# Kernel tuning notes

Hardware: AMD Instinct MI355X
Metric: run time of the kernel (lower is better)

The kernel has to match this reference:

```python
import jax, jax.numpy as jnp
import numpy as np

# config dims (see shape_source)
NO = 8        # Max_Object
NT = 32       # Max_Time
C = 512       # feat_dims
VD = 1024     # visual_dim
RD = 300      # self.nfeat (relation word-vector dim)
H = 4         # headnum
B = 8         # batch
No = NT * 2 * NO      # 512 object-graph nodes
Nr = NT * NO * NO     # 2048 relation-graph nodes


def _glorot(key, shape):
    fan_in = shape[0]
    return jax.random.normal(key, shape, dtype=jnp.float32) / np.sqrt(fan_in)


def setup_inputs() -> dict:
    key = jax.random.key(0)
    ks = jax.random.split(key, 18)
    inp = {
        "Ao": jax.random.uniform(ks[0], (B, No, No), dtype=jnp.float32),
        "srco": jax.random.normal(ks[1], (B, 1, 1, No, VD), dtype=jnp.float32),
        "Ar": jax.random.uniform(ks[2], (B, Nr, Nr), dtype=jnp.float32),
        "srcr": jax.random.normal(ks[3], (B, 1, 1, Nr, RD), dtype=jnp.float32),
        # GraphConvolution weights: gcl_o/gcl2_o and gcl_r/gcl2_r
        "Wo1": _glorot(ks[4], (VD, 1024)),
        "Wo2": _glorot(ks[5], (1024, C)),
        "Wr1": _glorot(ks[6], (RD, 1024)),
        "Wr2": _glorot(ks[7], (1024, C)),
        # MultiHeadAttention (e2n) projections
        "Wq": _glorot(ks[8], (C, C)), "bq": jnp.zeros((C,), jnp.float32),
        "Wk": _glorot(ks[9], (C, C)), "bk": jnp.zeros((C,), jnp.float32),
        "Wv": _glorot(ks[10], (C, C)), "bv": jnp.zeros((C,), jnp.float32),
        "Wp": _glorot(ks[11], (C, C)), "bp": jnp.zeros((C,), jnp.float32),
        # e2n_embed: Linear(2C -> C)
        "We": _glorot(ks[12], (2 * C, C)), "be": jnp.zeros((C,), jnp.float32),
    }
    return inp


def _gcn2(A, x, W1, W2):
    """Two stacked GraphConvolution layers with self-loops: relu((A+I) @ x @ W).
    A: (b,N,N), x: (b,N,Din). Vectorized over batch (torch code loops per-sample)."""
    eye = jnp.eye(A.shape[-1], dtype=A.dtype)
    Ah = A + eye
    h = jax.nn.relu(jnp.einsum('bij,bjd->bid', Ah, x @ W1))
    return jax.nn.relu(jnp.einsum('bij,bjd->bid', Ah, h @ W2))


def _mha(x, Wq, bq, Wk, bk, Wv, bv, Wp, bp):
    """Standard multi-head self-attention. x: (Bseg, S, C)."""
    Bs, S, _ = x.shape
    dh = C // H
    q = (x @ Wq + bq).reshape(Bs, S, H, dh)
    k = (x @ Wk + bk).reshape(Bs, S, H, dh)
    v = (x @ Wv + bv).reshape(Bs, S, H, dh)
    attn = jax.nn.softmax(jnp.einsum('bqhd,bkhd->bhqk', q, k) / np.sqrt(dh), axis=-1)
    o = jnp.einsum('bhqk,bkhd->bqhd', attn, v).reshape(Bs, S, C)
    return o @ Wp + bp


def _forward(Ao, srco, Ar, srcr, Wo1, Wo2, Wr1, Wr2,
             Wq, bq, Wk, bk, Wv, bv, Wp, bp, We, be):
    b = Ao.shape[0]
    # object-graph GCN (torch loops over batch; vectorized here)
    xo = srco[:, 0, 0, :, :VD]                       # (b, No, VD)
    srco_gcn = _gcn2(Ao, xo, Wo1, Wo2)               # (b, No, C)
    out_gcn_o = srco_gcn.reshape(b, NT, 2 * NO, C)
    # relation-graph GCN
    xr = srcr[:, 0, 0]                               # (b, Nr, RD)
    srcr_gcn = _gcn2(Ar, xr, Wr1, Wr2)               # (b, Nr, C)
    out_gcn_r = srcr_gcn.reshape(b, NT, NO * NO, C)
    # compute_e2n: segment-wise MHA over NO-token windows (torch loops over NO)
    r = out_gcn_r.reshape(b * NT, NO, NO, C)
    seg_a = r.reshape(b * NT * NO, NO, C)                      # rows of NOxNO grid
    a = _mha(seg_a, Wq, bq, Wk, bk, Wv, bv, Wp, bp).mean(axis=1)
    a = a.reshape(b * NT, NO, C)
    seg_o = jnp.swapaxes(r, 1, 2).reshape(b * NT * NO, NO, C)  # cols (permute 0,2,1,3)
    o = _mha(seg_o, Wq, bq, Wk, bk, Wv, bv, Wp, bp).mean(axis=1)
    o = o.reshape(b * NT, NO, C)
    tmp = jnp.concatenate([a, o], axis=1)                      # (b*NT, 2*NO, C)
    cat = jnp.concatenate([tmp, out_gcn_o.reshape(b * NT, 2 * NO, C)], axis=-1)
    out_e2n = cat @ We + be
    return out_e2n.reshape(b, NT, 2 * NO, C)


def reference(Ao, srco, Ar, srcr, Wo1, Wo2, Wr1, Wr2,
              Wq, bq, Wk, bk, Wv, bv, Wp, bp, We, be):
    return _forward(Ao, srco, Ar, srcr, Wo1, Wo2, Wr1, Wr2,
                    Wq, bq, Wk, bk, Wv, bv, Wp, bp, We, be)
```

## Files before the change

### kernel.cpp

```cpp
#include <hip/hip_runtime.h>
#include <hip/hip_bf16.h>


typedef __attribute__((ext_vector_type(4))) float f32x4;
typedef __attribute__((ext_vector_type(8))) short bf16x8s;

#define TILE 128
#define BKK 32
#define LDSS 40
#define LDSL 32

#if __has_builtin(__builtin_amdgcn_global_load_lds)
#define HAVE_GLL 1
#else
#define HAVE_GLL 0
#endif

__device__ inline void gll16(const __hip_bfloat16* g, __hip_bfloat16* l) {
#if HAVE_GLL
    __builtin_amdgcn_global_load_lds(
        (const __attribute__((address_space(1))) void*)g,
        (__attribute__((address_space(3))) void*)l,
        16, 0, 0);
#endif
}

__device__ inline void split2(float a, float b, unsigned& h, unsigned& l) {
    __hip_bfloat16 ha = __float2bfloat16(a), hb = __float2bfloat16(b);
    float ra = __bfloat162float(ha), rb = __bfloat162float(hb);
    __hip_bfloat16 la = __float2bfloat16(a - ra), lb = __float2bfloat16(b - rb);
    unsigned short uha = *(unsigned short*)&ha, uhb = *(unsigned short*)&hb;
    unsigned short ula = *(unsigned short*)&la, ulb = *(unsigned short*)&lb;
    h = (unsigned)uha | ((unsigned)uhb << 16);
    l = (unsigned)ula | ((unsigned)ulb << 16);
}

__device__ inline void splitw(float v, unsigned short& h, unsigned short& l) {
    __hip_bfloat16 hb = __float2bfloat16(v);
    __hip_bfloat16 lb = __float2bfloat16(v - __bfloat162float(hb));
    h = *(unsigned short*)&hb;
    l = *(unsigned short*)&lb;
}

__device__ inline void swz_block(int& bx, int& by, int& bz) {
    int gx = gridDim.x, gy = gridDim.y;
    int nwg = gx * gy * gridDim.z;
    int flat = bx + gx * (by + gy * bz);
    int cpx = nwg >> 3;
    int w = (flat & 7) * cpx + (flat >> 3);
    bx = w % gx;
    int t = w / gx;
    by = t % gy;
    bz = t / gy;
}

__global__ __launch_bounds__(256) void gemm_planes(
    const __hip_bfloat16* __restrict__ Aph, const __hip_bfloat16* __restrict__ Apl,
    long long sA, int lda,
    const __hip_bfloat16* __restrict__ BTh, const __hip_bfloat16* __restrict__ BTl,
    long long sBT, int ldbt,
    void* __restrict__ D, __hip_bfloat16* __restrict__ Dl_, long long sD, int ldd,
    const float* __restrict__ addN, long long sAddN, int ldaddN,
    const __hip_bfloat16* __restrict__ addTh, const __hip_bfloat16* __restrict__ addTl,
    long long sAddT, int ldaddT,
    const float* __restrict__ bias,
    int K, int relu, int outMode)
{
    __shared__ __hip_bfloat16 Ah[TILE * LDSL], Al[TILE * LDSL];
    __shared__ __hip_bfloat16 Bh[TILE * LDSL], Bl[TILE * LDSL];

    int bx = blockIdx.x, by = blockIdx.y, bz = blockIdx.z;
    swz_block(bx, by, bz);

    const int tid  = threadIdx.x;
    const int lane = tid & 63;
    const int wave = tid >> 6;
    const int wm   = (wave >> 1) * 64;
    const int wn   = (wave & 1) * 64;
    const int row0 = by * TILE;
    const int col0 = bx * TILE;
    const int b    = bz;

    const __hip_bfloat16* Abh = Aph + (size_t)b * sA;
    const __hip_bfloat16* Abl = Apl + (size_t)b * sA;
    const __hip_bfloat16* Bbh = BTh + (size_t)b * sBT;
    const __hip_bfloat16* Bbl = BTl + (size_t)b * sBT;

    f32x4 acc[4][4];
#pragma unroll
    for (int i = 0; i < 4; ++i)
#pragma unroll
        for (int j = 0; j < 4; ++j) acc[i][j] = (f32x4){0.f, 0.f, 0.f, 0.f};

    const int quad = lane >> 4;
    const int l16  = lane & 15;

    const int m0  = wave * 16 + (lane >> 2);
    const int m1  = (wave + 4) * 16 + (lane >> 2);
    const int sl  = lane & 3;
    const int kq0 = sl ^ ((m0 >> 1) & 3);
    const int kq1 = sl ^ ((m1 >> 1) & 3);
    const size_t gA0 = (size_t)(row0 + m0) * lda + kq0 * 8;
    const size_t gA1 = (size_t)(row0 + m1) * lda + kq1 * 8;
    const size_t gB0 = (size_t)(col0 + m0) * ldbt + kq0 * 8;
    const size_t gB1 = (size_t)(col0 + m1) * ldbt + kq1 * 8;
    const int ldsc0 = wave * 512;
    const int ldsc1 = (wave + 4) * 512;

    for (int k0 = 0; k0 < K; k0 += BKK) {
        __syncthreads();
#if HAVE_GLL
        gll16(Abh + gA0 + k0, &Ah[ldsc0]);
        gll16(Abh + gA1 + k0, &Ah[ldsc1]);
        gll16(Abl + gA0 + k0, &Al[ldsc0]);
        gll16(Abl + gA1 + k0, &Al[ldsc1]);
        gll16(Bbh + gB0 + k0, &Bh[ldsc0]);
        gll16(Bbh + gB1 + k0, &Bh[ldsc1]);
        gll16(Bbl + gB0 + k0, &Bl[ldsc0]);
        gll16(Bbl + gB1 + k0, &Bl[ldsc1]);
#else
        *(uint4*)(&Ah[m0 * LDSL + sl * 8]) = *(const uint4*)(Abh + gA0 + k0);
        *(uint4*)(&Ah[m1 * LDSL + sl * 8]) = *(const uint4*)(Abh + gA1 + k0);
        *(uint4*)(&Al[m0 * LDSL + sl * 8]) = *(const uint4*)(Abl + gA0 + k0);
        *(uint4*)(&Al[m1 * LDSL + sl * 8]) = *(const uint4*)(Abl + gA1 + k0);
        *(uint4*)(&Bh[m0 * LDSL + sl * 8]) = *(const uint4*)(Bbh + gB0 + k0);
        *(uint4*)(&Bh[m1 * LDSL + sl * 8]) = *(const uint4*)(Bbh + gB1 + k0);
        *(uint4*)(&Bl[m0 * LDSL + sl * 8]) = *(const uint4*)(Bbl + gB0 + k0);
        *(uint4*)(&Bl[m1 * LDSL + sl * 8]) = *(const uint4*)(Bbl + gB1 + k0);
#endif
        __syncthreads();

        bf16x8s bhf[4], blf[4];
#pragma unroll
        for (int nt = 0; nt < 4; ++nt) {
            int r = wn + nt * 16 + l16;
            int ss = (quad ^ ((r >> 1) & 3)) * 8;
            bhf[nt] = *(const bf16x8s*)(&Bh[r * LDSL + ss]);
            blf[nt] = *(const bf16x8s*)(&Bl[r * LDSL + ss]);
        }
#pragma unroll
        for (int mt = 0; mt < 4; ++mt) {
            int r = wm + mt * 16 + l16;
            int ss = (quad ^ ((r >> 1) & 3)) * 8;
            bf16x8s ahf = *(const bf16x8s*)(&Ah[r * LDSL + ss]);
            bf16x8s alf = *(const bf16x8s*)(&Al[r * LDSL + ss]);
#pragma unroll
            for (int nt = 0; nt < 4; ++nt) {
                acc[mt][nt] = __builtin_amdgcn_mfma_f32_16x16x32_bf16(ahf, bhf[nt], acc[mt][nt], 0, 0, 0);
                acc[mt][nt] = __builtin_amdgcn_mfma_f32_16x16x32_bf16(ahf, blf[nt], acc[mt][nt], 0, 0, 0);
                acc[mt][nt] = __builtin_amdgcn_mfma_f32_16x16x32_bf16(alf, bhf[nt], acc[mt][nt], 0, 0, 0);
            }
        }
    }

    float* DbF = (float*)D + (size_t)b * sD;
    __hip_bfloat16* Dhb = (__hip_bfloat16*)D + (size_t)b * sD;
    __hip_bfloat16* Dlb = Dl_ ? Dl_ + (size_t)b * sD : nullptr;
    const float* AddN = addN ? addN + (size_t)b * sAddN : nullptr;
    const __hip_bfloat16* ATh = addTh ? addTh + (size_t)b * sAddT : nullptr;
    const __hip_bfloat16* ATl = addTl ? addTl + (size_t)b * sAddT : nullptr;
#pragma unroll
    for (int mt = 0; mt < 4; ++mt)
#pragma unroll
        for (int nt = 0; nt < 4; ++nt)
#pragma unroll
            for (int r = 0; r < 4; ++r) {
                int m = row0 + wm + mt * 16 + quad * 4 + r;
                int n = col0 + wn + nt * 16 + l16;
                float v = acc[mt][nt][r];
                if (AddN) v += AddN[(size_t)m * ldaddN + n];
                if (ATh) v += __bfloat162float(ATh[(size_t)n * ldaddT + m])
                            + __bfloat162float(ATl[(size_t)n * ldaddT + m]);
                if (bias) v += bias[n];
                if (relu && v < 0.f) v = 0.f;
                if (outMode == 0) {
                    DbF[(size_t)m * ldd + n] = v;
                } else {
                    unsigned short hh, ll;
                    splitw(v, hh, ll);
                    size_t o = (size_t)m * ldd + n;
                    *(unsigned short*)&Dhb[o] = hh;
                    *(unsigned short*)&Dlb[o] = ll;
                }
            }
}

__global__ __launch_bounds__(256) void gemm_asplit(
    const float* __restrict__ A, long long sA, int lda,
    const __hip_bfloat16* __restrict__ BTh, const __hip_bfloat16* __restrict__ BTl,
    long long sBT, int ldbt,
    __hip_bfloat16* __restrict__ Dh_, __hip_bfloat16* __restrict__ Dl_,
    long long sD, int ldd,
    const float* __restrict__ addN, long long sAddN, int ldaddN,
    const __hip_bfloat16* __restrict__ addTh, const __hip_bfloat16* __restrict__ addTl,
    long long sAddT, int ldaddT,
    int K, int relu)
{
    __shared__ __hip_bfloat16 Ah[TILE * LDSS], Al[TILE * LDSS];
    __shared__ __hip_bfloat16 Bh[TILE * LDSS], Bl[TILE * LDSS];

    const int tid  = threadIdx.x;
    const int lane = tid & 63;
    const int wave = tid >> 6;
    const int wm   = (wave >> 1) * 64;
    const int wn   = (wave & 1) * 64;
    const int row0 = blockIdx.y * TILE;
    const int col0 = blockIdx.x * TILE;
    const int b    = blockIdx.z;

    const float* Ab = A + (size_t)b * sA;
    const __hip_bfloat16* Bbh = BTh + (size_t)b * sBT;
    const __hip_bfloat16* Bbl = BTl + (size_t)b * sBT;

    f32x4 acc[4][4];
#pragma unroll
    for (int i = 0; i < 4; ++i)
#pragma unroll
        for (int j = 0; j < 4; ++j) acc[i][j] = (f32x4){0.f, 0.f, 0.f, 0.f};

    const int quad = lane >> 4;
    const int l16  = lane & 15;

    for (int k0 = 0; k0 < K; k0 += BKK) {
        __syncthreads();
#pragma unroll
        for (int it = 0; it < 2; ++it) {
            int task = tid + it * 256;
            int m = task >> 2, kq = task & 3;
            const float* ap = Ab + (size_t)(row0 + m) * lda + k0 + kq * 8;
            float4 v0 = *(const float4*)ap;
            float4 v1 = *(const float4*)(ap + 4);
            uint4 H, L;
            split2(v0.x, v0.y, H.x, L.x); split2(v0.z, v0.w, H.y, L.y);
            split2(v1.x, v1.y, H.z, L.z); split2(v1.z, v1.w, H.w, L.w);
            *(uint4*)(&Ah[m * LDSS + kq * 8]) = H;
            *(uint4*)(&Al[m * LDSS + kq * 8]) = L;
        }
#pragma unroll
        for (int it = 0; it < 2; ++it) {
            int task = tid + it * 256;
            int n = task >> 2, kq = task & 3;
            size_t off = (size_t)(col0 + n) * ldbt + k0 + kq * 8;
            *(uint4*)(&Bh[n * LDSS + kq * 8]) = *(const uint4*)(Bbh + off);
            *(uint4*)(&Bl[n * LDSS + kq * 8]) = *(const uint4*)(Bbl + off);
        }
        __syncthreads();

        bf16x8s ah[4], al[4], bh[4], bl[4];
#pragma unroll
        for (int mt = 0; mt < 4; ++mt) {
            int r = (wm + mt * 16 + l16) * LDSS + quad * 8;
            ah[mt] = *(const bf16x8s*)(&Ah[r]);
            al[mt] = *(const bf16x8s*)(&Al[r]);
        }
#pragma unroll
        for (int nt = 0; nt < 4; ++nt) {
            int r = (wn + nt * 16 + l16) * LDSS + quad * 8;
            bh[nt] = *(const bf16x8s*)(&Bh[r]);
            bl[nt] = *(const bf16x8s*)(&Bl[r]);
        }
#pragma unroll
        for (int mt = 0; mt < 4; ++mt)
#pragma unroll
            for (int nt = 0; nt < 4; ++nt) {
                acc[mt][nt] = __builtin_amdgcn_mfma_f32_16x16x32_bf16(ah[mt], bh[nt], acc[mt][nt], 0, 0, 0);
                acc[mt][nt] = __builtin_amdgcn_mfma_f32_16x16x32_bf16(ah[mt], bl[nt], acc[mt][nt], 0, 0, 0);
                acc[mt][nt] = __builtin_amdgcn_mfma_f32_16x16x32_bf16(al[mt], bh[nt], acc[mt][nt], 0, 0, 0);
            }
    }

    __hip_bfloat16* Dhb = Dh_ + (size_t)b * sD;
    __hip_bfloat16* Dlb = Dl_ + (size_t)b * sD;
    const float* AddN = addN ? addN + (size_t)b * sAddN : nullptr;
    const __hip_bfloat16* ATh = addTh ? addTh + (size_t)b * sAddT : nullptr;
    const __hip_bfloat16* ATl = addTl ? addTl + (size_t)b * sAddT : nullptr;
#pragma unroll
    for (int mt = 0; mt < 4; ++mt)
#pragma unroll
        for (int nt = 0; nt < 4; ++nt)
#pragma unroll
            for (int r = 0; r < 4; ++r) {
                int m = row0 + wm + mt * 16 + quad * 4 + r;
                int n = col0 + wn + nt * 16 + l16;
                float v = acc[mt][nt][r];
                if (AddN) v += AddN[(size_t)m * ldaddN + n];
                if (ATh) v += __bfloat162float(ATh[(size_t)n * ldaddT + m])
                            + __bfloat162float(ATl[(size_t)n * ldaddT + m]);
                if (relu && v < 0.f) v = 0.f;
                unsigned short hh, ll;
                splitw(v, hh, ll);
                size_t o = (size_t)m * ldd + n;
                *(unsigned short*)&Dhb[o] = hh;
                *(unsigned short*)&Dlb[o] = ll;
            }
}

__global__ __launch_bounds__(256) void padtrans_split(
    const float* __restrict__ src,
    __hip_bfloat16* __restrict__ dsth, __hip_bfloat16* __restrict__ dstl,
    int R, int C, int Rp, int Cp)
{
    __shared__ float T[64][65];
    const int t = threadIdx.x;
    const int tr = t >> 4, tc = t & 15;
    const int c0 = blockIdx.x * 64, r0 = blockIdx.y * 64;
    const size_t bat = blockIdx.z;
    const float* sb = src + bat * (size_t)R * C;
    __hip_bfloat16* dhb = dsth + bat * (size_t)Cp * Rp;
    __hip_bfloat16* dlb = dstl + bat * (size_t)Cp * Rp;

#pragma unroll
    for (int i = 0; i < 4; ++i) {
        int rr = tr + i * 16;
        int gr = r0 + rr;
        float v0 = 0.f, v1 = 0.f, v2 = 0.f, v3 = 0.f;
        if (gr < R) {
            int c = c0 + tc * 4;
            const float* s = sb + (size_t)gr * C + c;
            if (c + 0 < C) v0 = s[0];
            if (c + 1 < C) v1 = s[1];
            if (c + 2 < C) v2 = s[2];
            if (c + 3 < C) v3 = s[3];
        }
        T[rr][tc * 4 + 0] = v0; T[rr][tc * 4 + 1] = v1;
        T[rr][tc * 4 + 2] = v2; T[rr][tc * 4 + 3] = v3;
    }
    __syncthreads();
#pragma unroll
    for (int i = 0; i < 4; ++i) {
        int cc = tr + i * 16;
        float4 v = { T[tc * 4 + 0][cc], T[tc * 4 + 1][cc],
                     T[tc * 4 + 2][cc], T[tc * 4 + 3][cc] };
        ushort4 H, L;
        splitw(v.x, H.x, L.x); splitw(v.y, H.y, L.y);
        splitw(v.z, H.z, L.z); splitw(v.w, H.w, L.w);
        size_t off = (size_t)(c0 + cc) * Rp + r0 + tc * 4;
        *(ushort4*)(dhb + off) = H;
        *(ushort4*)(dlb + off) = L;
    }
}

__global__ __launch_bounds__(256) void gemm_bf16(
    const __hip_bfloat16* __restrict__ A, long long sA, int lda,
    const __hip_bfloat16* __restrict__ B, long long sB, int ldb,
    void* __restrict__ D, long long sD, int ldd,
    const __hip_bfloat16* __restrict__ addsrc, long long sAdd, int ldadd,
    const float* __restrict__ bias,
    int K, int relu, int outF32)
{
    __shared__ __hip_bfloat16 As[TILE * LDSS];
    __shared__ __hip_bfloat16 Bs[TILE * LDSS];

    int bx = blockIdx.x, by = blockIdx.y, bz = blockIdx.z;
    swz_block(bx, by, bz);

    const int tid  = threadIdx.x;
    const int lane = tid & 63;
    const int wave = tid >> 6;
    const int wm   = (wave >> 1) * 64;
    const int wn   = (wave & 1) * 64;
    const int row0 = by * TILE;
    const int col0 = bx * TILE;
    const int b    = bz;

    const __hip_bfloat16* Ab = A + (size_t)b * sA;
    const __hip_bfloat16* Bb = B + (size_t)b * sB;

    f32x4 acc[4][4];
#pragma unroll
    for (int i = 0; i < 4; ++i)
#pragma unroll
        for (int j = 0; j < 4; ++j) acc[i][j] = (f32x4){0.f, 0.f, 0.f, 0.f};

    const int quad = lane >> 4;
    const int l16  = lane & 15;

    for (int k0 = 0; k0 < K; k0 += BKK) {
        __syncthreads();
#pragma unroll
        for (int it = 0; it < 2; ++it) {
            int task = tid + it * 256;
            int m = task >> 2, kq = task & 3;
            uint4 val = *(const uint4*)(Ab + (size_t)(row0 + m) * lda + k0 + kq * 8);
            *(uint4*)(&As[m * LDSS + kq * 8]) = val;
        }
#pragma unroll
        for (int it = 0; it < 2; ++it) {
            int task = tid + it * 256;
            int kk = task >> 4, n8 = task & 15;
            uint4 val = *(const uint4*)(Bb + (size_t)(k0 + kk) * ldb + col0 + n8 * 8);
            const __hip_bfloat16* v16 = (const __hip_bfloat16*)&val;
#pragma unroll
            for (int u = 0; u < 8; ++u)
                Bs[(n8 * 8 + u) * LDSS + kk] = v16[u];
        }
        __syncthreads();

        bf16x8s afrag[4], bfrag[4];
#pragma unroll
        for (int mt = 0; mt < 4; ++mt)
            afrag[mt] = *(const bf16x8s*)(&As[(wm + mt * 16 + l16) * LDSS + quad * 8]);
#pragma unroll
        for (int nt = 0; nt < 4; ++nt)
            bfrag[nt] = *(const bf16x8s*)(&Bs[(wn + nt * 16 + l16) * LDSS + quad * 8]);
#pragma unroll
        for (int mt = 0; mt < 4; ++mt)
#pragma unroll
            for (int nt = 0; nt < 4; ++nt)
                acc[mt][nt] = __builtin_amdgcn_mfma_f32_16x16x32_bf16(
                    afrag[mt], bfrag[nt], acc[mt][nt], 0, 0, 0);
    }

    __hip_bfloat16* Db16 = (__hip_bfloat16*)D + (size_t)b * sD;
    float*          DbF  = (float*)D + (size_t)b * sD;
    const __hip_bfloat16* Addb = addsrc ? addsrc + (size_t)b * sAdd : nullptr;
#pragma unroll
    for (int mt = 0; mt < 4; ++mt)
#pragma unroll
        for (int nt = 0; nt < 4; ++nt)
#pragma unroll
            for (int r = 0; r < 4; ++r) {
                int m = row0 + wm + mt * 16 + quad * 4 + r;
                int n = col0 + wn + nt * 16 + l16;
                float v = acc[mt][nt][r];
                if (Addb) v += __bfloat162float(Addb[(size_t)m * ldadd + n]);
                if (bias) v += bias[n];
                if (relu && v < 0.f) v = 0.f;
                if (outF32) DbF[(size_t)m * ldd + n] = v;
                else        Db16[(size_t)m * ldd + n] = __float2bfloat16(v);
            }
}

__global__ void convert_kernel(const float* __restrict__ src,
                               __hip_bfloat16* __restrict__ dst, int n4)
{
    int i = blockIdx.x * blockDim.x + threadIdx.x;
    if (i >= n4) return;
    float4 v = ((const float4*)src)[i];
    __hip_bfloat16 t0 = __float2bfloat16(v.x), t1 = __float2bfloat16(v.y);
    __hip_bfloat16 t2 = __float2bfloat16(v.z), t3 = __float2bfloat16(v.w);
    ushort4 o = { *(unsigned short*)&t0, *(unsigned short*)&t1,
                  *(unsigned short*)&t2, *(unsigned short*)&t3 };
    ((ushort4*)dst)[i] = o;
}

__global__ void split_kernel(const float* __restrict__ src,
                             __hip_bfloat16* __restrict__ dh,
                             __hip_bfloat16* __restrict__ dl, int n4)
{
    int i = blockIdx.x * blockDim.x + threadIdx.x;
    if (i >= n4) return;
    float4 v = ((const float4*)src)[i];
    ushort4 H, L;
    splitw(v.x, H.x, L.x); splitw(v.y, H.y, L.y);
    splitw(v.z, H.z, L.z); splitw(v.w, H.w, L.w);
    ((ushort4*)dh)[i] = H;
    ((ushort4*)dl)[i] = L;
}

__global__ __launch_bounds__(256) void attn_kernel(
    const float* __restrict__ q,
    const float* __restrict__ k,
    const float* __restrict__ v,
    __hip_bfloat16* __restrict__ abar)
{
    __shared__ float qs[8][512], ks[8][512], vs[8][512];
    __shared__ float sc[4][8][8];
    __shared__ float wb[4][8];

    const int tid  = threadIdx.x;
    const int mode = blockIdx.y;
    const int g    = blockIdx.x >> 3;
    const int idx  = blockIdx.x & 7;
    const int rowBase = g * 64;

    for (int t = tid; t < 512; t += 256) {
        int p = t >> 6, c8 = (t & 63) * 8;
        int row = (mode == 0) ? (rowBase + idx * 8 + p) : (rowBase + p * 8 + idx);
        const float* qp = q + (size_t)row * 512 + c8;
        const float* kp = k + (size_t)row * 512 + c8;
        const float* vp = v + (size_t)row * 512 + c8;
        *(float4*)(&qs[p][c8])     = *(const float4*)(qp);
        *(float4*)(&qs[p][c8 + 4]) = *(const float4*)(qp + 4);
        *(float4*)(&ks[p][c8])     = *(const float4*)(kp);
        *(float4*)(&ks[p][c8 + 4]) = *(const float4*)(kp + 4);
        *(float4*)(&vs[p][c8])     = *(const float4*)(vp);
        *(float4*)(&vs[p][c8 + 4]) = *(const float4*)(vp + 4);
    }
    __syncthreads();

    {
        int h = tid >> 6, l = tid & 63;
        int i = l >> 3, j = l & 7;
        const float* qrow = &qs[i][h * 128];
        const float* krow = &ks[j][h * 128];
        float s = 0.f;
#pragma unroll
        for (int d = 0; d < 128; d += 4) {
            float4 qa = *(const float4*)(qrow + d);
            float4 kb = *(const float4*)(krow + d);
            s += qa.x * kb.x + qa.y * kb.y + qa.z * kb.z + qa.w * kb.w;
        }
        sc[h][i][j] = s * 0.08838834764831845f;
    }
    __syncthreads();

    if (tid < 32) {
        int h = tid >> 3, i = tid & 7;
        float mx = -1e30f;
#pragma unroll
        for (int j = 0; j < 8; ++j) mx = fmaxf(mx, sc[h][i][j]);
        float e[8], sum = 0.f;
#pragma unroll
        for (int j = 0; j < 8; ++j) { e[j] = __expf(sc[h][i][j] - mx); sum += e[j]; }
        float inv = 1.f / sum;
#pragma unroll
        for (int j = 0; j < 8; ++j) sc[h][i][j] = e[j] * inv;
    }
    __syncthreads();

    if (tid < 32) {
        int h = tid >> 3, j = tid & 7;
        float s = 0.f;
#pragma unroll
        for (int i = 0; i < 8; ++i) s += sc[h][i][j];
        wb[h][j] = s * 0.125f;
    }
    __syncthreads();

    {
        int orow = g * 16 + mode * 8 + idx;
        for (int c = tid; c < 512; c += 256) {
            int h = c >> 7;
            float o = 0.f;
#pragma unroll
            for (int j = 0; j < 8; ++j) o += wb[h][j] * vs[j][c];
            abar[(size_t)orow * 512 + c] = __float2bfloat16(o);
        }
    }
}


extern "C" void kernel_launch(void* const* d_in, const int* in_sizes, int n_in,
                              void* d_out, int out_size, void* d_ws, size_t ws_size,
                              hipStream_t stream)
{
    const float* Ao   = (const float*)d_in[0];
    const float* srco = (const float*)d_in[1];
    const float* Ar   = (const float*)d_in[2];
    const float* srcr = (const float*)d_in[3];
    const float* Wo1  = (const float*)d_in[4];
    const float* Wo2  = (const float*)d_in[5];
    const float* Wr1  = (const float*)d_in[6];
    const float* Wr2  = (const float*)d_in[7];
    const float* Wq   = (const float*)d_in[8];
    const float* bq   = (const float*)d_in[9];
    const float* Wk   = (const float*)d_in[10];
    const float* bk   = (const float*)d_in[11];
    const float* Wv   = (const float*)d_in[12];
    const float* bv   = (const float*)d_in[13];
    const float* Wp   = (const float*)d_in[14];
    const float* bp   = (const float*)d_in[15];
    const float* We   = (const float*)d_in[16];
    const float* be   = (const float*)d_in[17];
    float* out = (float*)d_out;

    char* ws = (char*)d_ws;
    const size_t R0 = 0;
    const size_t R1 = 67108864;
    const size_t R2 = 100663296;
    const size_t R3 = 134217728;
    const size_t R4 = 167772160;
    const size_t R5 = 192937984;
    const size_t R6 = 199491584;

    __hip_bfloat16* HRh = (__hip_bfloat16*)(ws + R0);
    __hip_bfloat16* HRl = HRh + 16777216;
    float* qF   = (float*)(ws + R0);
    float* kF   = (float*)(ws + R0 + 33554432);
    float* T2Rf = (float*)(ws + R1);
    float* vF   = (float*)(ws + R1);
    __hip_bfloat16* Uh = (__hip_bfloat16*)(ws + R2);
    __hip_bfloat16* Ul = Uh + 6291456;
    __hip_bfloat16* T2RTh = (__hip_bfloat16*)(ws + R2);
    __hip_bfloat16* T2RTl = T2RTh + 8388608;
    __hip_bfloat16* GRh = (__hip_bfloat16*)(ws + R3);
    __hip_bfloat16* GRl = GRh + 8388608;
    __hip_bfloat16* XPTh = (__hip_bfloat16*)(ws + R4);
    __hip_bfloat16* XPTl = XPTh + 6291456;
    __hip_bfloat16* ABAR = (__hip_bfloat16*)(ws + R4);
    __hip_bfloat16* WPTh = (__hip_bfloat16*)(ws + R5);
    __hip_bfloat16* WPTl = WPTh + 327680;
    __hip_bfloat16* Wr2Th = (__hip_bfloat16*)(ws + R5 + 1310720);
    __hip_bfloat16* Wr2Tl = Wr2Th + 524288;
    __hip_bfloat16* WqTh = (__hip_bfloat16*)(ws + R5 + 3407872);
    __hip_bfloat16* WqTl = WqTh + 262144;
    __hip_bfloat16* WkTh = (__hip_bfloat16*)(ws + R5 + 4456448);
    __hip_bfloat16* WkTl = WkTh + 262144;
    __hip_bfloat16* WvTh = (__hip_bfloat16*)(ws + R5 + 5505024);
    __hip_bfloat16* WvTl = WvTh + 262144;
    __hip_bfloat16* Arh = (__hip_bfloat16*)(ws + R6);
    __hip_bfloat16* Arl = Arh + 33554432;
    const bool haveArPlanes = ws_size >= R6 + 2ull * 67108864ull;

    __hip_bfloat16* TO    = (__hip_bfloat16*)(ws + R2 + 0);
    __hip_bfloat16* HO    = (__hip_bfloat16*)(ws + R2 + 8388608);
    __hip_bfloat16* T2O   = (__hip_bfloat16*)(ws + R2 + 16777216);
    __hip_bfloat16* CAT   = (__hip_bfloat16*)(ws + R2 + 20971520);
    __hip_bfloat16* srcoB = (__hip_bfloat16*)(ws + R2 + 29360128);
    __hip_bfloat16* AoB   = (__hip_bfloat16*)(ws + R2 + 37748736);
    __hip_bfloat16* Wo1B  = (__hip_bfloat16*)(ws + R2 + 41943040);
    __hip_bfloat16* Wo2B  = (__hip_bfloat16*)(ws + R2 + 44040192);
    __hip_bfloat16* WeB   = (__hip_bfloat16*)(ws + R2 + 45088768);
    __hip_bfloat16* WpB   = (__hip_bfloat16*)(ws + R2 + 46137344);

    dim3 blk(256);
    auto cvt = [&](const float* s, __hip_bfloat16* d, int n) {
        convert_kernel<<<dim3((n / 4 + 255) / 256), blk, 0, stream>>>(s, d, n / 4);
    };

    padtrans_split<<<dim3(6, 32, 8), blk, 0, stream>>>(srcr, XPTh, XPTl, 2048, 300, 2048, 384);
    padtrans_split<<<dim3(16, 5, 1), blk, 0, stream>>>(Wr1, WPTh, WPTl, 300, 1024, 320, 1024);
    padtrans_split<<<dim3(8, 16, 1), blk, 0, stream>>>(Wr2, Wr2Th, Wr2Tl, 1024, 512, 1024, 512);
    padtrans_split<<<dim3(8, 8, 1), blk, 0, stream>>>(Wq, WqTh, WqTl, 512, 512, 512, 512);
    padtrans_split<<<dim3(8, 8, 1), blk, 0, stream>>>(Wk, WkTh, WkTl, 512, 512, 512, 512);
    padtrans_split<<<dim3(8, 8, 1), blk, 0, stream>>>(Wv, WvTh, WvTl, 512, 512, 512, 512);

    if (haveArPlanes) {
        split_kernel<<<dim3(32768), blk, 0, stream>>>(Ar, Arh, Arl, 8388608);
        gemm_planes<<<dim3(3, 16, 8), blk, 0, stream>>>(
            Arh, Arl, 2048LL * 2048, 2048, XPTh, XPTl, 384LL * 2048, 2048,
            Uh, Ul, 2048LL * 384, 384,
            nullptr, 0, 0, XPTh, XPTl, 384LL * 2048, 2048,
            nullptr, 2048, 0, 1);
    } else {
        gemm_asplit<<<dim3(3, 16, 8), blk, 0, stream>>>(
            Ar, 2048LL * 2048, 2048, XPTh, XPTl, 384LL * 2048, 2048,
            Uh, Ul, 2048LL * 384, 384,
            nullptr, 0, 0, XPTh, XPTl, 384LL * 2048, 2048,
            2048, 0);
    }
    gemm_planes<<<dim3(8, 128, 1), blk, 0, stream>>>(
        Uh, Ul, 0, 384, WPTh, WPTl, 0, 320,
        HRh, HRl, 0, 1024,
        nullptr, 0, 0, nullptr, nullptr, 0, 0,
        nullptr, 320, 1, 1);
    gemm_planes<<<dim3(4, 128, 1), blk, 0, stream>>>(
        HRh, HRl, 0, 1024, Wr2Th, Wr2Tl, 0, 1024,
        T2Rf, nullptr, 0, 512,
        nullptr, 0, 0, nullptr, nullptr, 0, 0,
        nullptr, 1024, 0, 0);
    padtrans_split<<<dim3(8, 32, 8), blk, 0, stream>>>(T2Rf, T2RTh, T2RTl, 2048, 512, 2048, 512);
    if (haveArPlanes) {
        gemm_planes<<<dim3(4, 16, 8), blk, 0, stream>>>(
            Arh, Arl, 2048LL * 2048, 2048, T2RTh, T2RTl, 512LL * 2048, 2048,
            GRh, GRl, 2048LL * 512, 512,
            T2Rf, 2048LL * 512, 512, nullptr, nullptr, 0, 0,
            nullptr, 2048, 1, 1);
    } else {
        gemm_asplit<<<dim3(4, 16, 8), blk, 0, stream>>>(
            Ar, 2048LL * 2048, 2048, T2RTh, T2RTl, 512LL * 2048, 2048,
            GRh, GRl, 2048LL * 512, 512,
            T2Rf, 2048LL * 512, 512, nullptr, nullptr, 0, 0,
            2048, 1);
    }
    gemm_planes<<<dim3(4, 128, 1), blk, 0, stream>>>(
        GRh, GRl, 0, 512, WqTh, WqTl, 0, 512,
        qF, nullptr, 0, 512,
        nullptr, 0, 0, nullptr, nullptr, 0, 0,
        bq, 512, 0, 0);
    gemm_planes<<<dim3(4, 128, 1), blk, 0, stream>>>(
        GRh, GRl, 0, 512, WkTh, WkTl, 0, 512,
        kF, nullptr, 0, 512,
        nullptr, 0, 0, nullptr, nullptr, 0, 0,
        bk, 512, 0, 0);
    gemm_planes<<<dim3(4, 128, 1), blk, 0, stream>>>(
        GRh, GRl, 0, 512, WvTh, WvTl, 0, 512,
        vF, nullptr, 0, 512,
        nullptr, 0, 0, nullptr, nullptr, 0, 0,
        bv, 512, 0, 0);
    attn_kernel<<<dim3(2048, 2), blk, 0, stream>>>(qF, kF, vF, ABAR);

    cvt(srco, srcoB, 4194304);
    cvt(Ao, AoB, 2097152);
    cvt(Wo1, Wo1B, 1048576);
    cvt(Wo2, Wo2B, 524288);
    cvt(We, WeB, 524288);
    cvt(Wp, WpB, 262144);
    gemm_bf16<<<dim3(8, 32, 1), blk, 0, stream>>>(srcoB, 0, 1024, Wo1B, 0, 1024,
        TO, 0, 1024, nullptr, 0, 0, nullptr, 1024, 0, 0);
    gemm_bf16<<<dim3(8, 4, 8), blk, 0, stream>>>(AoB, 512LL * 512, 512, TO, 512LL * 1024, 1024,
        HO, 512LL * 1024, 1024, TO, 512LL * 1024, 1024, nullptr, 512, 1, 0);
    gemm_bf16<<<dim3(4, 32, 1), blk, 0, stream>>>(HO, 0, 1024, Wo2B, 0, 512,
        T2O, 0, 512, nullptr, 0, 0, nullptr, 1024, 0, 0);
    gemm_bf16<<<dim3(4, 4, 8), blk, 0, stream>>>(AoB, 512LL * 512, 512, T2O, 512LL * 512, 512,
        (void*)(CAT + 512), 512LL * 1024, 1024, T2O, 512LL * 512, 512, nullptr, 512, 1, 0);
    gemm_bf16<<<dim3(4, 32, 1), blk, 0, stream>>>(ABAR, 0, 512, WpB, 0, 512,
        CAT, 0, 1024, nullptr, 0, 0, bp, 512, 0, 0);
    gemm_bf16<<<dim3(4, 32, 1), blk, 0, stream>>>(CAT, 0, 1024, WeB, 0, 512,
        out, 0, 512, nullptr, 0, 0, be, 1024, 0, 1);
}
```

Before: 1.150 ms.

## Double-buffer LDS tiles in gemm_planes to prefetch next K slice during MFMA

The split-bf16 GEMM kernel now keeps two LDS buffers per operand plane. It issues the loads for the next K tile right after the barrier, then runs MFMAs on the current tile, and drops one of the two barriers per iteration. The goal is to hide global-to-LDS load latency behind the matrix math. In exchange, LDS per block doubles to 64 KB, which lowers how many blocks can be resident per CU. Correctness also depends on the barrier waiting for the asynchronous global-to-LDS loads.

```diff
diff --git a/kernel.cpp b/kernel.cpp
--- a/kernel.cpp
+++ b/kernel.cpp
@@ -66,8 +66,8 @@
     const float* __restrict__ bias,
     int K, int relu, int outMode)
 {
-    __shared__ __hip_bfloat16 Ah[TILE * LDSL], Al[TILE * LDSL];
-    __shared__ __hip_bfloat16 Bh[TILE * LDSL], Bl[TILE * LDSL];
+    __shared__ __hip_bfloat16 AhB[2][TILE * LDSL], AlB[2][TILE * LDSL];
+    __shared__ __hip_bfloat16 BhB[2][TILE * LDSL], BlB[2][TILE * LDSL];
 
     int bx = blockIdx.x, by = blockIdx.y, bz = blockIdx.z;
     swz_block(bx, by, bz);
@@ -107,36 +107,52 @@
     const int ldsc0 = wave * 512;
     const int ldsc1 = (wave + 4) * 512;
 
-    for (int k0 = 0; k0 < K; k0 += BKK) {
+#if HAVE_GLL
+#define STAGE(buf, kk) do { \
+    gll16(Abh + gA0 + (kk), &AhB[buf][ldsc0]); \
+    gll16(Abh + gA1 + (kk), &AhB[buf][ldsc1]); \
+    gll16(Abl + gA0 + (kk), &AlB[buf][ldsc0]); \
+    gll16(Abl + gA1 + (kk), &AlB[buf][ldsc1]); \
+    gll16(Bbh + gB0 + (kk), &BhB[buf][ldsc0]); \
+    gll16(Bbh + gB1 + (kk), &BhB[buf][ldsc1]); \
+    gll16(Bbl + gB0 + (kk), &BlB[buf][ldsc0]); \
+    gll16(Bbl + gB1 + (kk), &BlB[buf][ldsc1]); \
+} while (0)
+#else
+#define STAGE(buf, kk) do { \
+    *(uint4*)(&AhB[buf][m0 * LDSL + sl * 8]) = *(const uint4*)(Abh + gA0 + (kk)); \
+    *(uint4*)(&AhB[buf][m1 * LDSL + sl * 8]) = *(const uint4*)(Abh + gA1 + (kk)); \
+    *(uint4*)(&AlB[buf][m0 * LDSL + sl * 8]) = *(const uint4*)(Abl + gA0 + (kk)); \
+    *(uint4*)(&AlB[buf][m1 * LDSL + sl * 8]) = *(const uint4*)(Abl + gA1 + (kk)); \
+    *(uint4*)(&BhB[buf][m0 * LDSL + sl * 8]) = *(const uint4*)(Bbh + gB0 + (kk)); \
+    *(uint4*)(&BhB[buf][m1 * LDSL + sl * 8]) = *(const uint4*)(Bbh + gB1 + (kk)); \
+    *(uint4*)(&BlB[buf][m0 * LDSL + sl * 8]) = *(const uint4*)(Bbl + gB0 + (kk)); \
+    *(uint4*)(&BlB[buf][m1 * LDSL + sl * 8]) = *(const uint4*)(Bbl + gB1 + (kk)); \
+} while (0)
+#endif
+
+    const int nt = K / BKK;
+    int cur = 0;
+
+    STAGE(0, 0);
+
+    for (int t = 0; t < nt; ++t) {
         __syncthreads();
-#if HAVE_GLL
-        gll16(Abh + gA0 + k0, &Ah[ldsc0]);
-        gll16(Abh + gA1 + k0, &Ah[ldsc1]);
-        gll16(Abl + gA0 + k0, &Al[ldsc0]);
-        gll16(Abl + gA1 + k0, &Al[ldsc1]);
-        gll16(Bbh + gB0 + k0, &Bh[ldsc0]);
-        gll16(Bbh + gB1 + k0, &Bh[ldsc1]);
-        gll16(Bbl + gB0 + k0, &Bl[ldsc0]);
-        gll16(Bbl + gB1 + k0, &Bl[ldsc1]);
-#else
-        *(uint4*)(&Ah[m0 * LDSL + sl * 8]) = *(const uint4*)(Abh + gA0 + k0);
-        *(uint4*)(&Ah[m1 * LDSL + sl * 8]) = *(const uint4*)(Abh + gA1 + k0);
-        *(uint4*)(&Al[m0 * LDSL + sl * 8]) = *(const uint4*)(Abl + gA0 + k0);
-        *(uint4*)(&Al[m1 * LDSL + sl * 8]) = *(const uint4*)(Abl + gA1 + k0);
-        *(uint4*)(&Bh[m0 * LDSL + sl * 8]) = *(const uint4*)(Bbh + gB0 + k0);
-        *(uint4*)(&Bh[m1 * LDSL + sl * 8]) = *(const uint4*)(Bbh + gB1 + k0);
-        *(uint4*)(&Bl[m0 * LDSL + sl * 8]) = *(const uint4*)(Bbl + gB0 + k0);
-        *(uint4*)(&Bl[m1 * LDSL + sl * 8]) = *(const uint4*)(Bbl + gB1 + k0);
-#endif
-        __syncthreads();
+
+        if (t + 1 < nt) STAGE(cur ^ 1, (t + 1) * BKK);
+
+        const __hip_bfloat16* Ah = AhB[cur];
+        const __hip_bfloat16* Al = AlB[cur];
+        const __hip_bfloat16* Bh = BhB[cur];
+        const __hip_bfloat16* Bl = BlB[cur];
 
         bf16x8s bhf[4], blf[4];
 #pragma unroll
-        for (int nt = 0; nt < 4; ++nt) {
-            int r = wn + nt * 16 + l16;
+        for (int nt2 = 0; nt2 < 4; ++nt2) {
+            int r = wn + nt2 * 16 + l16;
             int ss = (quad ^ ((r >> 1) & 3)) * 8;
-            bhf[nt] = *(const bf16x8s*)(&Bh[r * LDSL + ss]);
-            blf[nt] = *(const bf16x8s*)(&Bl[r * LDSL + ss]);
+            bhf[nt2] = *(const bf16x8s*)(&Bh[r * LDSL + ss]);
+            blf[nt2] = *(const bf16x8s*)(&Bl[r * LDSL + ss]);
         }
 #pragma unroll
         for (int mt = 0; mt < 4; ++mt) {
@@ -145,13 +161,15 @@
             bf16x8s ahf = *(const bf16x8s*)(&Ah[r * LDSL + ss]);
             bf16x8s alf = *(const bf16x8s*)(&Al[r * LDSL + ss]);
 #pragma unroll
-            for (int nt = 0; nt < 4; ++nt) {
-                acc[mt][nt] = __builtin_amdgcn_mfma_f32_16x16x32_bf16(ahf, bhf[nt], acc[mt][nt], 0, 0, 0);
-                acc[mt][nt] = __builtin_amdgcn_mfma_f32_16x16x32_bf16(ahf, blf[nt], acc[mt][nt], 0, 0, 0);
-                acc[mt][nt] = __builtin_amdgcn_mfma_f32_16x16x32_bf16(alf, bhf[nt], acc[mt][nt], 0, 0, 0);
+            for (int nt2 = 0; nt2 < 4; ++nt2) {
+                acc[mt][nt2] = __builtin_amdgcn_mfma_f32_16x16x32_bf16(ahf, bhf[nt2], acc[mt][nt2], 0, 0, 0);
+                acc[mt][nt2] = __builtin_amdgcn_mfma_f32_16x16x32_bf16(ahf, blf[nt2], acc[mt][nt2], 0, 0, 0);
+                acc[mt][nt2] = __builtin_amdgcn_mfma_f32_16x16x32_bf16(alf, bhf[nt2], acc[mt][nt2], 0, 0, 0);
             }
         }
-    }
+        cur ^= 1;
+    }
+#undef STAGE
 
     float* DbF = (float*)D + (size_t)b * sD;
     __hip_bfloat16* Dhb = (__hip_bfloat16*)D + (size_t)b * sD;
@@ -162,12 +180,12 @@
 #pragma unroll
     for (int mt = 0; mt < 4; ++mt)
 #pragma unroll
-        for (int nt = 0; nt < 4; ++nt)
+        for (int nt2 = 0; nt2 < 4; ++nt2)
 #pragma unroll
             for (int r = 0; r < 4; ++r) {
                 int m = row0 + wm + mt * 16 + quad * 4 + r;
-                int n = col0 + wn + nt * 16 + l16;
-                float v = acc[mt][nt][r];
+                int n = col0 + wn + nt2 * 16 + l16;
+                float v = acc[mt][nt2][r];
                 if (AddN) v += AddN[(size_t)m * ldaddN + n];
                 if (ATh) v += __bfloat162float(ATh[(size_t)n * ldaddT + m])
                             + __bfloat162float(ATl[(size_t)n * ldaddT + m]);
```

New measurement: 1.132 ms. Within noise of the previous version (-1.6%).
